# Kernel optimization log

Hardware: AMD Instinct MI355X
Metric: run time of the kernel (lower is better)

## Reference

```python
import jax, jax.numpy as jnp
import numpy as np

B, N, D = 16, 2048, 64

def setup_inputs() -> dict:
    key = jax.random.key(0)
    kq, kk, kv = jax.random.split(key, 3)
    queries = jax.random.normal(kq, (B, N, D), dtype=jnp.float32)
    keys = jax.random.normal(kk, (B, N, D), dtype=jnp.float32)
    values = jax.random.normal(kv, (B, N, D), dtype=jnp.float32)
    scaling_factor = jnp.asarray(np.sqrt(D), dtype=jnp.float32)
    return {"queries": queries, "keys": keys, "values": values, "scaling_factor": scaling_factor}

def reference(queries, keys, values, scaling_factor):
    # scores: [B, N, N] = Q K^T / scale
    scores = jnp.einsum('bqd,bkd->bqk', queries, keys) / scaling_factor
    atn = jax.nn.softmax(scores, axis=2)
    return jnp.einsum('bqk,bkd->bqd', atn, values)
```

## Files before the change

kernel.cpp:

```cpp
#include <hip/hip_runtime.h>
#include <hip/hip_bf16.h>

#define BATCH 16
#define SEQ 2048
#define DIM 64
#define TQ 64
#define KT 128
#define KP 72
#define VP 152

typedef __attribute__((ext_vector_type(8))) __bf16 bf16x8;
typedef __attribute__((ext_vector_type(8))) unsigned short u16x8;
typedef __attribute__((ext_vector_type(4))) float f32x4;

#if __has_builtin(__builtin_amdgcn_exp2f)
#define EXP2F(x) __builtin_amdgcn_exp2f(x)
#else
#define EXP2F(x) __expf(0.69314718055994531f * (x))
#endif

__device__ __forceinline__ unsigned short f2bf(float f) {
    union { float f; unsigned int u; } v; v.f = f;
    unsigned int r = v.u + 0x7fffu + ((v.u >> 16) & 1u);
    return (unsigned short)(r >> 16);
}

__device__ __forceinline__ bf16x8 ld_bf8(const unsigned short* p) {
    u16x8 u = *(const u16x8*)p;
    return __builtin_bit_cast(bf16x8, u);
}

__global__ __launch_bounds__(256)
void preconvert_qk(const float* __restrict__ Q, const float* __restrict__ K,
                   const float* __restrict__ scaling,
                   unsigned short* __restrict__ Qs, unsigned short* __restrict__ Ks) {
    const float c = 1.4426950408889634f / scaling[0];
    const size_t i = ((size_t)blockIdx.x * 256 + threadIdx.x) * 8;
    float4 a0 = *(const float4*)(Q + i);
    float4 a1 = *(const float4*)(Q + i + 4);
    u16x8 qo;
    qo[0] = f2bf(a0.x * c); qo[1] = f2bf(a0.y * c); qo[2] = f2bf(a0.z * c); qo[3] = f2bf(a0.w * c);
    qo[4] = f2bf(a1.x * c); qo[5] = f2bf(a1.y * c); qo[6] = f2bf(a1.z * c); qo[7] = f2bf(a1.w * c);
    *(u16x8*)(Qs + i) = qo;
    float4 b0 = *(const float4*)(K + i);
    float4 b1 = *(const float4*)(K + i + 4);
    u16x8 ko;
    ko[0] = f2bf(b0.x); ko[1] = f2bf(b0.y); ko[2] = f2bf(b0.z); ko[3] = f2bf(b0.w);
    ko[4] = f2bf(b1.x); ko[5] = f2bf(b1.y); ko[6] = f2bf(b1.z); ko[7] = f2bf(b1.w);
    *(u16x8*)(Ks + i) = ko;
}

__global__ __launch_bounds__(256)
void preconvert_v(const float* __restrict__ V, unsigned short* __restrict__ Vts) {
    __shared__ float vt[KT * 65];
    const int tid = threadIdx.x;
    const int b  = blockIdx.x >> 4;
    const int kt = (blockIdx.x & 15) * KT;
    const float* src = V + ((size_t)(b * SEQ + kt)) * DIM;
    #pragma unroll
    for (int p = 0; p < 8; ++p) {
        const int f = p * 256 + tid;
        const int row = f >> 4, c4 = (f & 15) << 2;
        float4 x = *(const float4*)(src + row * DIM + c4);
        vt[row * 65 + c4 + 0] = x.x; vt[row * 65 + c4 + 1] = x.y;
        vt[row * 65 + c4 + 2] = x.z; vt[row * 65 + c4 + 3] = x.w;
    }
    __syncthreads();
    #pragma unroll
    for (int p = 0; p < 4; ++p) {
        const int cid = p * 256 + tid;
        const int d = cid >> 4, kc = cid & 15;
        u16x8 o;
        #pragma unroll
        for (int j = 0; j < 8; ++j) o[j] = f2bf(vt[(kc * 8 + j) * 65 + d]);
        *(u16x8*)(Vts + ((size_t)(b * DIM + d)) * SEQ + kt + kc * 8) = o;
    }
}

__global__ __launch_bounds__(256, 2)
void attn_flash_kernel(const unsigned short* __restrict__ Qs,
                       const unsigned short* __restrict__ Ks,
                       const unsigned short* __restrict__ Vts,
                       float* __restrict__ O) {
    __shared__ unsigned short Klds[KT * KP];
    __shared__ unsigned short Vtlds[DIM * VP];
    __shared__ unsigned short Plds[4 * 16 * VP];

    const int tid  = threadIdx.x;
    const int w    = tid >> 6;
    const int lane = tid & 63;
    const int lo   = lane & 15;
    const int quad = lane >> 4;

    const int b  = blockIdx.x >> 5;
    const int q0 = (blockIdx.x & 31) * TQ;

    bf16x8 aq[2];
    {
        const unsigned short* qsrc = Qs + ((size_t)(b * SEQ + q0 + w * 16 + lo)) * DIM;
        aq[0] = ld_bf8(qsrc + quad * 8);
        aq[1] = ld_bf8(qsrc + 32 + quad * 8);
    }

    f32x4 Oacc[4];
    #pragma unroll
    for (int dt = 0; dt < 4; ++dt) Oacc[dt] = f32x4{0.f, 0.f, 0.f, 0.f};
    float psum[4] = {0.f, 0.f, 0.f, 0.f};

    unsigned short* pw = &Plds[w * 16 * VP];

    for (int kt = 0; kt < SEQ; kt += KT) {
        __syncthreads();
        {
            const unsigned short* kbase = Ks + ((size_t)(b * SEQ + kt)) * DIM;
            #pragma unroll
            for (int p = 0; p < 4; ++p) {
                const int cid = p * 256 + tid;
                const int key = cid >> 3, ch = cid & 7;
                *(u16x8*)&Klds[key * KP + ch * 8] = *(const u16x8*)(kbase + key * DIM + ch * 8);
            }
        }
        {
            const unsigned short* vbase = Vts + (size_t)b * DIM * SEQ + kt;
            #pragma unroll
            for (int p = 0; p < 4; ++p) {
                const int cid = p * 256 + tid;
                const int d = cid >> 4, ch = cid & 15;
                *(u16x8*)&Vtlds[d * VP + ch * 8] = *(const u16x8*)(vbase + (size_t)d * SEQ + ch * 8);
            }
        }
        __syncthreads();

        f32x4 S[8];
        #pragma unroll
        for (int t = 0; t < 8; ++t) {
            S[t] = f32x4{0.f, 0.f, 0.f, 0.f};
            #pragma unroll
            for (int c = 0; c < 2; ++c) {
                bf16x8 bk = ld_bf8(&Klds[(t * 16 + lo) * KP + c * 32 + quad * 8]);
                S[t] = __builtin_amdgcn_mfma_f32_16x16x32_bf16(aq[c], bk, S[t], 0, 0, 0);
            }
        }

        #pragma unroll
        for (int t = 0; t < 8; ++t) {
            #pragma unroll
            for (int r = 0; r < 4; ++r) {
                float p = EXP2F(S[t][r]);
                psum[r] += p;
                pw[(quad * 4 + r) * VP + t * 16 + lo] = f2bf(p);
            }
        }

        #pragma unroll
        for (int c = 0; c < 4; ++c) {
            bf16x8 pa = ld_bf8(&pw[lo * VP + c * 32 + quad * 8]);
            #pragma unroll
            for (int dt = 0; dt < 4; ++dt) {
                bf16x8 bv = ld_bf8(&Vtlds[(dt * 16 + lo) * VP + c * 32 + quad * 8]);
                Oacc[dt] = __builtin_amdgcn_mfma_f32_16x16x32_bf16(pa, bv, Oacc[dt], 0, 0, 0);
            }
        }
    }

    #pragma unroll
    for (int r = 0; r < 4; ++r) {
        float l = psum[r];
        #pragma unroll
        for (int off = 1; off < 16; off <<= 1) l += __shfl_xor(l, off);
        const float invl = 1.0f / l;
        const int row = quad * 4 + r;
        float* orow = O + ((size_t)(b * SEQ + q0 + w * 16 + row)) * DIM;
        #pragma unroll
        for (int dt = 0; dt < 4; ++dt)
            orow[dt * 16 + lo] = Oacc[dt][r] * invl;
    }
}

extern "C" void kernel_launch(void* const* d_in, const int* in_sizes, int n_in,
                              void* d_out, int out_size, void* d_ws, size_t ws_size,
                              hipStream_t stream) {
    const float* Q = (const float*)d_in[0];
    const float* K = (const float*)d_in[1];
    const float* V = (const float*)d_in[2];
    const float* scaling = (const float*)d_in[3];
    float* O = (float*)d_out;

    const size_t NELEM = (size_t)BATCH * SEQ * DIM;
    unsigned short* Qs  = (unsigned short*)d_ws;
    unsigned short* Ks  = Qs + NELEM;
    unsigned short* Vts = Ks + NELEM;

    preconvert_qk<<<dim3(NELEM / (256 * 8)), dim3(256), 0, stream>>>(Q, K, scaling, Qs, Ks);
    preconvert_v<<<dim3(BATCH * (SEQ / KT)), dim3(256), 0, stream>>>(V, Vts);
    attn_flash_kernel<<<dim3(BATCH * (SEQ / TQ)), dim3(256), 0, stream>>>(Qs, Ks, Vts, O);
}
```

Baseline: 119.3 us.

## Switch attention to 32x32x16 MFMA with two-wave blocks and fused preconversion

The attention kernel moves from 16x16x32 to 32x32x16 bf16 MFMA, with each of two waves per block owning 32 query rows instead of four waves owning 16. LDS paddings are retuned and P is written using a hardware bf16 convert. The Q/K and V preconversion kernels are merged into one launch. The aim is fewer MFMA and LDS instructions per FLOP and one less launch, at the cost of half as many threads per block, each doing more staging loads, and higher register pressure.

Result: slower. 122.1 us (+2.4%).

```diff
diff --git a/kernel.cpp b/kernel.cpp
--- a/kernel.cpp
+++ b/kernel.cpp
@@ -7,11 +7,12 @@
 #define TQ 64
 #define KT 128
 #define KP 72
-#define VP 152
+#define VPP 136
+#define PP 136
 
 typedef __attribute__((ext_vector_type(8))) __bf16 bf16x8;
 typedef __attribute__((ext_vector_type(8))) unsigned short u16x8;
-typedef __attribute__((ext_vector_type(4))) float f32x4;
+typedef __attribute__((ext_vector_type(16))) float f32x16;
 
 #if __has_builtin(__builtin_amdgcn_exp2f)
 #define EXP2F(x) __builtin_amdgcn_exp2f(x)
@@ -25,97 +26,107 @@
     return (unsigned short)(r >> 16);
 }
 
+__device__ __forceinline__ unsigned short f2bf_hw(float f) {
+    __bf16 h = (__bf16)f;
+    return __builtin_bit_cast(unsigned short, h);
+}
+
 __device__ __forceinline__ bf16x8 ld_bf8(const unsigned short* p) {
     u16x8 u = *(const u16x8*)p;
     return __builtin_bit_cast(bf16x8, u);
 }
 
 __global__ __launch_bounds__(256)
-void preconvert_qk(const float* __restrict__ Q, const float* __restrict__ K,
-                   const float* __restrict__ scaling,
-                   unsigned short* __restrict__ Qs, unsigned short* __restrict__ Ks) {
-    const float c = 1.4426950408889634f / scaling[0];
-    const size_t i = ((size_t)blockIdx.x * 256 + threadIdx.x) * 8;
-    float4 a0 = *(const float4*)(Q + i);
-    float4 a1 = *(const float4*)(Q + i + 4);
-    u16x8 qo;
-    qo[0] = f2bf(a0.x * c); qo[1] = f2bf(a0.y * c); qo[2] = f2bf(a0.z * c); qo[3] = f2bf(a0.w * c);
-    qo[4] = f2bf(a1.x * c); qo[5] = f2bf(a1.y * c); qo[6] = f2bf(a1.z * c); qo[7] = f2bf(a1.w * c);
-    *(u16x8*)(Qs + i) = qo;
-    float4 b0 = *(const float4*)(K + i);
-    float4 b1 = *(const float4*)(K + i + 4);
-    u16x8 ko;
-    ko[0] = f2bf(b0.x); ko[1] = f2bf(b0.y); ko[2] = f2bf(b0.z); ko[3] = f2bf(b0.w);
-    ko[4] = f2bf(b1.x); ko[5] = f2bf(b1.y); ko[6] = f2bf(b1.z); ko[7] = f2bf(b1.w);
-    *(u16x8*)(Ks + i) = ko;
-}
-
-__global__ __launch_bounds__(256)
-void preconvert_v(const float* __restrict__ V, unsigned short* __restrict__ Vts) {
-    __shared__ float vt[KT * 65];
+void preconvert_all(const float* __restrict__ Q, const float* __restrict__ K,
+                    const float* __restrict__ V, const float* __restrict__ scaling,
+                    unsigned short* __restrict__ Qs, unsigned short* __restrict__ Ks,
+                    unsigned short* __restrict__ Vts) {
     const int tid = threadIdx.x;
-    const int b  = blockIdx.x >> 4;
-    const int kt = (blockIdx.x & 15) * KT;
-    const float* src = V + ((size_t)(b * SEQ + kt)) * DIM;
-    #pragma unroll
-    for (int p = 0; p < 8; ++p) {
-        const int f = p * 256 + tid;
-        const int row = f >> 4, c4 = (f & 15) << 2;
-        float4 x = *(const float4*)(src + row * DIM + c4);
-        vt[row * 65 + c4 + 0] = x.x; vt[row * 65 + c4 + 1] = x.y;
-        vt[row * 65 + c4 + 2] = x.z; vt[row * 65 + c4 + 3] = x.w;
-    }
-    __syncthreads();
-    #pragma unroll
-    for (int p = 0; p < 4; ++p) {
-        const int cid = p * 256 + tid;
-        const int d = cid >> 4, kc = cid & 15;
-        u16x8 o;
-        #pragma unroll
-        for (int j = 0; j < 8; ++j) o[j] = f2bf(vt[(kc * 8 + j) * 65 + d]);
-        *(u16x8*)(Vts + ((size_t)(b * DIM + d)) * SEQ + kt + kc * 8) = o;
-    }
-}
-
-__global__ __launch_bounds__(256, 2)
+    if (blockIdx.x < 1024) {
+        const float c = 1.4426950408889634f / scaling[0];
+        const size_t i = ((size_t)blockIdx.x * 256 + tid) * 8;
+        float4 a0 = *(const float4*)(Q + i);
+        float4 a1 = *(const float4*)(Q + i + 4);
+        u16x8 qo;
+        qo[0] = f2bf(a0.x * c); qo[1] = f2bf(a0.y * c); qo[2] = f2bf(a0.z * c); qo[3] = f2bf(a0.w * c);
+        qo[4] = f2bf(a1.x * c); qo[5] = f2bf(a1.y * c); qo[6] = f2bf(a1.z * c); qo[7] = f2bf(a1.w * c);
+        *(u16x8*)(Qs + i) = qo;
+        float4 b0 = *(const float4*)(K + i);
+        float4 b1 = *(const float4*)(K + i + 4);
+        u16x8 ko;
+        ko[0] = f2bf(b0.x); ko[1] = f2bf(b0.y); ko[2] = f2bf(b0.z); ko[3] = f2bf(b0.w);
+        ko[4] = f2bf(b1.x); ko[5] = f2bf(b1.y); ko[6] = f2bf(b1.z); ko[7] = f2bf(b1.w);
+        *(u16x8*)(Ks + i) = ko;
+    } else {
+        __shared__ float vt[KT * 65];
+        const int vb = blockIdx.x - 1024;
+        const int b  = vb >> 4;
+        const int kt = (vb & 15) * KT;
+        const float* src = V + ((size_t)(b * SEQ + kt)) * DIM;
+        #pragma unroll
+        for (int p = 0; p < 8; ++p) {
+            const int f = p * 256 + tid;
+            const int row = f >> 4, c4 = (f & 15) << 2;
+            float4 x = *(const float4*)(src + row * DIM + c4);
+            vt[row * 65 + c4 + 0] = x.x; vt[row * 65 + c4 + 1] = x.y;
+            vt[row * 65 + c4 + 2] = x.z; vt[row * 65 + c4 + 3] = x.w;
+        }
+        __syncthreads();
+        #pragma unroll
+        for (int p = 0; p < 4; ++p) {
+            const int cid = p * 256 + tid;
+            const int d = cid >> 4, kc = cid & 15;
+            u16x8 o;
+            #pragma unroll
+            for (int j = 0; j < 8; ++j) o[j] = f2bf(vt[(kc * 8 + j) * 65 + d]);
+            *(u16x8*)(Vts + ((size_t)(b * DIM + d)) * SEQ + kt + kc * 8) = o;
+        }
+    }
+}
+
+__global__ __launch_bounds__(128, 2)
 void attn_flash_kernel(const unsigned short* __restrict__ Qs,
                        const unsigned short* __restrict__ Ks,
                        const unsigned short* __restrict__ Vts,
                        float* __restrict__ O) {
     __shared__ unsigned short Klds[KT * KP];
-    __shared__ unsigned short Vtlds[DIM * VP];
-    __shared__ unsigned short Plds[4 * 16 * VP];
+    __shared__ unsigned short Vtlds[DIM * VPP];
+    __shared__ unsigned short Plds[2 * 32 * PP];
 
     const int tid  = threadIdx.x;
     const int w    = tid >> 6;
     const int lane = tid & 63;
-    const int lo   = lane & 15;
-    const int quad = lane >> 4;
+    const int m    = lane & 31;
+    const int h    = lane >> 5;
 
     const int b  = blockIdx.x >> 5;
     const int q0 = (blockIdx.x & 31) * TQ;
 
-    bf16x8 aq[2];
+    bf16x8 aq[4];
     {
-        const unsigned short* qsrc = Qs + ((size_t)(b * SEQ + q0 + w * 16 + lo)) * DIM;
-        aq[0] = ld_bf8(qsrc + quad * 8);
-        aq[1] = ld_bf8(qsrc + 32 + quad * 8);
-    }
-
-    f32x4 Oacc[4];
+        const unsigned short* qsrc = Qs + ((size_t)(b * SEQ + q0 + w * 32 + m)) * DIM;
+        #pragma unroll
+        for (int c = 0; c < 4; ++c) aq[c] = ld_bf8(qsrc + c * 16 + h * 8);
+    }
+
+    f32x16 Oacc[2];
     #pragma unroll
-    for (int dt = 0; dt < 4; ++dt) Oacc[dt] = f32x4{0.f, 0.f, 0.f, 0.f};
-    float psum[4] = {0.f, 0.f, 0.f, 0.f};
-
-    unsigned short* pw = &Plds[w * 16 * VP];
+    for (int dt = 0; dt < 2; ++dt)
+        #pragma unroll
+        for (int r = 0; r < 16; ++r) Oacc[dt][r] = 0.f;
+    float psum[16];
+    #pragma unroll
+    for (int r = 0; r < 16; ++r) psum[r] = 0.f;
+
+    unsigned short* pw = &Plds[w * 32 * PP];
 
     for (int kt = 0; kt < SEQ; kt += KT) {
         __syncthreads();
         {
             const unsigned short* kbase = Ks + ((size_t)(b * SEQ + kt)) * DIM;
             #pragma unroll
-            for (int p = 0; p < 4; ++p) {
-                const int cid = p * 256 + tid;
+            for (int p = 0; p < 8; ++p) {
+                const int cid = p * 128 + tid;
                 const int key = cid >> 3, ch = cid & 7;
                 *(u16x8*)&Klds[key * KP + ch * 8] = *(const u16x8*)(kbase + key * DIM + ch * 8);
             }
@@ -123,57 +134,55 @@
         {
             const unsigned short* vbase = Vts + (size_t)b * DIM * SEQ + kt;
             #pragma unroll
-            for (int p = 0; p < 4; ++p) {
-                const int cid = p * 256 + tid;
+            for (int p = 0; p < 8; ++p) {
+                const int cid = p * 128 + tid;
                 const int d = cid >> 4, ch = cid & 15;
-                *(u16x8*)&Vtlds[d * VP + ch * 8] = *(const u16x8*)(vbase + (size_t)d * SEQ + ch * 8);
+                *(u16x8*)&Vtlds[d * VPP + ch * 8] = *(const u16x8*)(vbase + (size_t)d * SEQ + ch * 8);
             }
         }
         __syncthreads();
 
-        f32x4 S[8];
-        #pragma unroll
-        for (int t = 0; t < 8; ++t) {
-            S[t] = f32x4{0.f, 0.f, 0.f, 0.f};
-            #pragma unroll
-            for (int c = 0; c < 2; ++c) {
-                bf16x8 bk = ld_bf8(&Klds[(t * 16 + lo) * KP + c * 32 + quad * 8]);
-                S[t] = __builtin_amdgcn_mfma_f32_16x16x32_bf16(aq[c], bk, S[t], 0, 0, 0);
-            }
-        }
-
-        #pragma unroll
-        for (int t = 0; t < 8; ++t) {
-            #pragma unroll
-            for (int r = 0; r < 4; ++r) {
-                float p = EXP2F(S[t][r]);
+        #pragma unroll
+        for (int t = 0; t < 4; ++t) {
+            f32x16 S;
+            #pragma unroll
+            for (int r = 0; r < 16; ++r) S[r] = 0.f;
+            #pragma unroll
+            for (int c = 0; c < 4; ++c) {
+                bf16x8 bk = ld_bf8(&Klds[(t * 32 + m) * KP + c * 16 + h * 8]);
+                S = __builtin_amdgcn_mfma_f32_32x32x16_bf16(aq[c], bk, S, 0, 0, 0);
+            }
+            #pragma unroll
+            for (int r = 0; r < 16; ++r) {
+                float p = EXP2F(S[r]);
                 psum[r] += p;
-                pw[(quad * 4 + r) * VP + t * 16 + lo] = f2bf(p);
-            }
-        }
-
-        #pragma unroll
-        for (int c = 0; c < 4; ++c) {
-            bf16x8 pa = ld_bf8(&pw[lo * VP + c * 32 + quad * 8]);
-            #pragma unroll
-            for (int dt = 0; dt < 4; ++dt) {
-                bf16x8 bv = ld_bf8(&Vtlds[(dt * 16 + lo) * VP + c * 32 + quad * 8]);
-                Oacc[dt] = __builtin_amdgcn_mfma_f32_16x16x32_bf16(pa, bv, Oacc[dt], 0, 0, 0);
+                const int row = (r & 3) + 8 * (r >> 2) + 4 * h;
+                pw[row * PP + t * 32 + m] = f2bf_hw(p);
+            }
+        }
+
+        #pragma unroll
+        for (int kc = 0; kc < 8; ++kc) {
+            bf16x8 pa = ld_bf8(&pw[m * PP + kc * 16 + h * 8]);
+            #pragma unroll
+            for (int dt = 0; dt < 2; ++dt) {
+                bf16x8 bv = ld_bf8(&Vtlds[(dt * 32 + m) * VPP + kc * 16 + h * 8]);
+                Oacc[dt] = __builtin_amdgcn_mfma_f32_32x32x16_bf16(pa, bv, Oacc[dt], 0, 0, 0);
             }
         }
     }
 
     #pragma unroll
-    for (int r = 0; r < 4; ++r) {
+    for (int r = 0; r < 16; ++r) {
         float l = psum[r];
         #pragma unroll
-        for (int off = 1; off < 16; off <<= 1) l += __shfl_xor(l, off);
+        for (int off = 1; off < 32; off <<= 1) l += __shfl_xor(l, off);
         const float invl = 1.0f / l;
-        const int row = quad * 4 + r;
-        float* orow = O + ((size_t)(b * SEQ + q0 + w * 16 + row)) * DIM;
-        #pragma unroll
-        for (int dt = 0; dt < 4; ++dt)
-            orow[dt * 16 + lo] = Oacc[dt][r] * invl;
+        const int row = (r & 3) + 8 * (r >> 2) + 4 * h;
+        float* orow = O + ((size_t)(b * SEQ + q0 + w * 32 + row)) * DIM;
+        #pragma unroll
+        for (int dt = 0; dt < 2; ++dt)
+            orow[dt * 32 + m] = Oacc[dt][r] * invl;
     }
 }
 
@@ -191,7 +200,6 @@
     unsigned short* Ks  = Qs + NELEM;
     unsigned short* Vts = Ks + NELEM;
 
-    preconvert_qk<<<dim3(NELEM / (256 * 8)), dim3(256), 0, stream>>>(Q, K, scaling, Qs, Ks);
-    preconvert_v<<<dim3(BATCH * (SEQ / KT)), dim3(256), 0, stream>>>(V, Vts);
-    attn_flash_kernel<<<dim3(BATCH * (SEQ / TQ)), dim3(256), 0, stream>>>(Qs, Ks, Vts, O);
-}
+    preconvert_all<<<dim3(1024 + BATCH * (SEQ / KT)), dim3(256), 0, stream>>>(Q, K, V, scaling, Qs, Ks, Vts);
+    attn_flash_kernel<<<dim3(BATCH * (SEQ / TQ)), dim3(128), 0, stream>>>(Qs, Ks, Vts, O);
+}
```
